# Kernel tuning notes

Hardware: AMD Instinct MI355X
Metric: run time of the kernel (lower is better)

Reference implementation:

```python
import jax, jax.numpy as jnp
import numpy as np

N_NODES = 50000
N_EDGES = 800000
N_GRAPHS = 500
NFEAT = 128
NHID = 64
NLAYER = 3
BN_EPS = 1e-5


def setup_inputs() -> dict:
    key = jax.random.key(0)
    ks = jax.random.split(key, 8)
    x = jax.random.normal(ks[0], (N_NODES, NFEAT), dtype=jnp.float32)
    edge_index = jax.random.randint(ks[1], (2, N_EDGES), 0, N_NODES)
    batch = jnp.sort(jax.random.randint(ks[2], (N_NODES,), 0, N_GRAPHS))
    Wt = jax.random.normal(ks[3], (NFEAT, NHID), dtype=jnp.float32) / np.float32(np.sqrt(NFEAT))
    bt = jnp.zeros((NHID,), jnp.float32)
    gamma0 = jnp.ones((NHID,), jnp.float32)
    beta0 = jnp.zeros((NHID,), jnp.float32)
    W1 = jax.random.normal(ks[4], (NLAYER, NHID, NHID), dtype=jnp.float32) / np.float32(np.sqrt(NHID))
    W2 = jax.random.normal(ks[5], (NLAYER, NHID, NHID), dtype=jnp.float32) / np.float32(np.sqrt(NHID))
    gammas = jnp.ones((NLAYER, NHID), jnp.float32)
    betas = jnp.zeros((NLAYER, NHID), jnp.float32)
    return dict(x=x, edge_index=edge_index, batch=batch, Wt=Wt, bt=bt,
                gamma0=gamma0, beta0=beta0, W1=W1, W2=W2, gammas=gammas, betas=betas)


def _bn(h, g, b):
    # BatchNorm1d training-mode math: batch mean, biased variance
    mean = jnp.mean(h, axis=0)
    var = jnp.mean((h - mean) ** 2, axis=0)
    return (h - mean) * jax.lax.rsqrt(var + BN_EPS) * g + b


def _pool_mean(h, batch):
    s = jax.ops.segment_sum(h, batch, num_segments=N_GRAPHS)
    cnt = jax.ops.segment_sum(jnp.ones((h.shape[0], 1), h.dtype), batch, num_segments=N_GRAPHS)
    return s / jnp.maximum(cnt, 1.0)


def _embed_std(h, batch):
    m = _pool_mean(h, batch)                      # [G, nhid]
    s = jnp.sqrt(_pool_mean((h - m[batch]) ** 2, batch))
    return m, s


def reference(x, edge_index, batch, Wt, bt, gamma0, beta0, W1, W2, gammas, betas):
    src, dst = edge_index[0], edge_index[1]
    h = _bn(x @ Wt + bt, gamma0, beta0)           # transform: Linear + BN
    e0, s0 = _embed_std(h, batch)

    def step(h, p):
        w1, w2, g, b = p
        agg = jax.ops.segment_sum(h[src], dst, num_segments=N_NODES)  # GIN sum-aggregation
        z = (h + agg)                              # (1+eps)*x + agg, eps=0
        z = jax.nn.relu(z @ w1) @ w2               # GINConv nn: Linear-ReLU-Linear (no bias)
        z = _bn(jax.nn.relu(z), g, b)              # act then BN
        e, s = _embed_std(z, batch)
        return z, (e, s)

    _, (es, ss) = jax.lax.scan(step, h, (W1, W2, gammas, betas))
    graph_embeds = jnp.concatenate([e0[None], es], axis=0)  # [nlayer+1, G, nhid]
    graph_stds = jnp.concatenate([s0[None], ss], axis=0)
    return graph_embeds, graph_stds
```

## Files before the change

### kernel.cpp

```cpp
#include <hip/hip_runtime.h>
#include <hip/hip_bf16.h>

#define NN 50000
#define NE 800000
#define NG 500
#define NF 128
#define NH 64
#define NB 256
#define NPB 196
#define EPB 4096
#define NBLK ((NE + EPB - 1)/EPB)
#define CSR_LDS 2048

typedef unsigned int u32;
typedef unsigned short u16;
typedef _Float16 h2 __attribute__((ext_vector_type(2)));
typedef _Float16 h8 __attribute__((ext_vector_type(8)));
typedef float f32x4 __attribute__((ext_vector_type(4)));

__device__ __forceinline__ float bf1(u16 v){ return __uint_as_float(((u32)v) << 16); }
__device__ __forceinline__ float h1(u16 v){ return (float)__builtin_bit_cast(_Float16, v); }
__device__ __forceinline__ u32 pk(float a, float b){
  return __builtin_bit_cast(u32, __builtin_amdgcn_cvt_pkrtz(a, b));
}
__device__ __forceinline__ h2 uph(u32 u){ return __builtin_bit_cast(h2, u); }
__device__ __forceinline__ u16 f16b(float f){ return __builtin_bit_cast(u16, (_Float16)f); }

__device__ __forceinline__ void cv8h(uint4 q, float* f){
  h2 v0 = uph(q.x), v1 = uph(q.y), v2 = uph(q.z), v3 = uph(q.w);
  f[0]=(float)v0.x; f[1]=(float)v0.y; f[2]=(float)v1.x; f[3]=(float)v1.y;
  f[4]=(float)v2.x; f[5]=(float)v2.y; f[6]=(float)v3.x; f[7]=(float)v3.y;
}

__device__ __forceinline__ h8 pack8(float4 p, float4 q){
  uint4 t;
  t.x = pk(p.x, p.y); t.y = pk(p.z, p.w);
  t.z = pk(q.x, q.y); t.w = pk(q.z, q.w);
  return __builtin_bit_cast(h8, t);
}
__device__ __forceinline__ f32x4 z4(){
  f32x4 v; v[0]=0.f; v[1]=0.f; v[2]=0.f; v[3]=0.f; return v;
}

__global__ __launch_bounds__(256) void k_init(const u32* __restrict__ xw, int* __restrict__ flag,
    const int* __restrict__ batch, int* __restrict__ starts,
    const float* __restrict__ Wt, const float* __restrict__ W1, const float* __restrict__ W2,
    u16* __restrict__ wtT, u16* __restrict__ w1T, u16* __restrict__ w2T){
  int b = blockIdx.x, tid = threadIdx.x;
  if (b < 48){
    int t = b*256 + tid;
    if (t < NH*NF){
      int c = t >> 7, k = t & 127;
      wtT[t] = f16b(Wt[(size_t)k*NH + c]);
    }
    if (t < 3*NH*NH){
      int l = t >> 12, c = (t >> 6) & 63, k = t & 63;
      w1T[t] = f16b(W1[(size_t)l*NH*NH + k*NH + c]);
      w2T[t] = f16b(W2[(size_t)l*NH*NH + k*NH + c]);
    }
  } else {
    if (tid < 64){
      u32 w = xw[tid];
      u32 lo = w & 0xFFFFu;
      u32 e = (lo >> 7) & 0xFFu;
      bool vote = (e >= 0x60u && e <= 0x8Fu);
      unsigned long long m = __ballot(vote);
      if (tid == 0) flag[0] = (__popcll(m) >= 32) ? 1 : 0;
    }
    for (int g = tid; g <= NG; g += 256){
      int lo = 0, hi = NN;
      while (lo < hi){ int mid = (lo + hi) >> 1; if (batch[mid] < g) lo = mid + 1; else hi = mid; }
      starts[g] = lo;
    }
  }
}


__global__ __launch_bounds__(256) void k_bhist(const int* __restrict__ ei, int* __restrict__ bcount,
    int* __restrict__ bstart, int* __restrict__ bcur, int* __restrict__ ticket){
  __shared__ int h[NB];
  __shared__ int part[NB];
  __shared__ int isLast;
  int tid = threadIdx.x;
  h[tid] = 0;
  __syncthreads();
  int e0 = blockIdx.x*EPB;
  #pragma unroll
  for (int i = 0; i < 16; i++){
    int e = e0 + i*256 + tid;
    if (e < NE) atomicAdd(&h[ei[NE + e] / NPB], 1);
  }
  __syncthreads();
  if (h[tid]) atomicAdd(&bcount[tid], h[tid]);
  __threadfence();
  if (tid == 0) isLast = (atomicAdd(ticket, 1) == (int)gridDim.x - 1);
  __syncthreads();
  if (!isLast) return;
  int v = atomicAdd(&bcount[tid], 0);
  part[tid] = v;
  __syncthreads();
  for (int off = 1; off < 256; off <<= 1){
    int u = (tid >= off) ? part[tid-off] : 0;
    __syncthreads();
    part[tid] += u;
    __syncthreads();
  }
  int ex = part[tid] - v;
  bstart[tid] = ex;
  bcur[tid] = ex;
  if (tid == 0) bstart[NB] = NE;
}

__global__ __launch_bounds__(256) void k_bscat(const int* __restrict__ ei,
    int* __restrict__ bcur, u32* __restrict__ pkE){
  __shared__ int h[NB];
  __shared__ int loff[NB];
  __shared__ int base[NB];
  __shared__ int part[NB];
  __shared__ u32 sv[EPB];
  int tid = threadIdx.x;
  h[tid] = 0;
  __syncthreads();
  int e0 = blockIdx.x*EPB;
  u32 meta[16], vals[16];
  #pragma unroll
  for (int i = 0; i < 16; i++){
    int e = e0 + i*256 + tid;
    if (e < NE){
      int s = ei[e], d = ei[NE + e];
      int b = d / NPB;
      int r = atomicAdd(&h[b], 1);
      meta[i] = ((u32)b << 16) | (u32)r;
      vals[i] = ((u32)d << 16) | (u32)s;
    } else meta[i] = 0xFFFFFFFFu;
  }
  __syncthreads();
  int cnt = h[tid];
  part[tid] = cnt;
  __syncthreads();
  for (int off = 1; off < 256; off <<= 1){
    int u = (tid >= off) ? part[tid-off] : 0;
    __syncthreads();
    part[tid] += u;
    __syncthreads();
  }
  loff[tid] = part[tid] - cnt;
  base[tid] = cnt ? atomicAdd(&bcur[tid], cnt) : 0;
  __syncthreads();
  #pragma unroll
  for (int i = 0; i < 16; i++){
    if (meta[i] != 0xFFFFFFFFu){
      int b = meta[i] >> 16, r = meta[i] & 0xFFFFu;
      sv[loff[b] + r] = vals[i];
    }
  }
  __syncthreads();
  int total = min(EPB, NE - e0);
  for (int j = tid; j < total; j += 256){
    u32 v = sv[j];
    int b = (int)(v >> 16) / NPB;
    pkE[base[b] + (j - loff[b])] = v;
  }
}

__global__ __launch_bounds__(256) void k_bfill(const u32* __restrict__ pkE,
    const int* __restrict__ bstart, int* __restrict__ rowptr, int* __restrict__ csr){
  __shared__ int part[NB];
  __shared__ int cur[NB];
  int b = blockIdx.x;
  int tid = threadIdx.x;
  int nb0 = b*NPB;
  int nr = min(NPB, NN - nb0);
  int rbeg = bstart[b], rend = bstart[b+1];
  part[tid] = 0;
  __syncthreads();
  for (int j = rbeg + tid; j < rend; j += 256){
    u32 pe = pkE[j];
    atomicAdd(&part[(int)(pe >> 16) - nb0], 1);
  }
  __syncthreads();
  int v = part[tid];
  __syncthreads();
  for (int off = 1; off < 256; off <<= 1){
    int u = (tid >= off) ? part[tid-off] : 0;
    __syncthreads();
    part[tid] += u;
    __syncthreads();
  }
  int ex = part[tid] - v;
  if (tid < nr) rowptr[nb0 + tid] = rbeg + ex;
  if (b == NB-1 && tid == 0) rowptr[NN] = NE;
  cur[tid] = ex;
  __syncthreads();
  for (int j = rbeg + tid; j < rend; j += 256){
    u32 pe = pkE[j];
    int node = (int)(pe >> 16) - nb0;
    int p = atomicAdd(&cur[node], 1);
    csr[rbeg + p] = (int)(pe & 0xFFFFu);
  }
}

__global__ __launch_bounds__(256) void k_transform_m(const float* __restrict__ x,
    const u16* __restrict__ wtT, const float* __restrict__ bt,
    u16* __restrict__ th, float* __restrict__ s1){
  __shared__ float sRed[8*NH];
  int tid = threadIdx.x;
  int w = tid >> 6, l = tid & 63;
  int lr = l & 15, kb = l >> 4;
  h8 bf[4][4];
  #pragma unroll
  for (int n = 0; n < 4; n++)
    #pragma unroll
    for (int kk = 0; kk < 4; kk++)
      bf[n][kk] = *(const h8*)&wtT[(size_t)(16*n + lr)*NF + kk*32 + kb*8];
  int node0 = blockIdx.x*64 + w*16;
  int rowA = node0 + lr; if (rowA > NN-1) rowA = NN-1;
  const float* xr = x + (size_t)rowA*NF + kb*8;
  f32x4 acc[4];
  #pragma unroll
  for (int n = 0; n < 4; n++) acc[n] = z4();
  #pragma unroll
  for (int kk = 0; kk < 4; kk++){
    float4 p = *(const float4*)(xr + kk*32);
    float4 q = *(const float4*)(xr + kk*32 + 4);
    h8 a = pack8(p, q);
    #pragma unroll
    for (int n = 0; n < 4; n++)
      acc[n] = __builtin_amdgcn_mfma_f32_16x16x32_f16(a, bf[n][kk], acc[n], 0, 0, 0);
  }
  #pragma unroll
  for (int n = 0; n < 4; n++){
    float bias = bt[16*n + lr];
    float a1 = 0.f, a2 = 0.f;
    #pragma unroll
    for (int r = 0; r < 4; r++){
      int g = node0 + 4*kb + r;
      float v = acc[n][r] + bias;
      if (g < NN){
        th[(size_t)g*NH + 16*n + lr] = f16b(v);
        a1 += v; a2 += v*v;
      }
    }
    a1 += __shfl_xor(a1, 16); a1 += __shfl_xor(a1, 32);
    a2 += __shfl_xor(a2, 16); a2 += __shfl_xor(a2, 32);
    if (kb == 0){
      sRed[w*NH + 16*n + lr] = a1;
      sRed[(4+w)*NH + 16*n + lr] = a2;
    }
  }
  __syncthreads();
  if (tid < NH){
    float a1 = sRed[tid] + sRed[NH+tid] + sRed[2*NH+tid] + sRed[3*NH+tid];
    float a2 = sRed[4*NH+tid] + sRed[5*NH+tid] + sRed[6*NH+tid] + sRed[7*NH+tid];
    unsafeAtomicAdd(&s1[tid], a1);
    unsafeAtomicAdd(&s1[NH+tid], a2);
  }
}

__global__ __launch_bounds__(512) void k_gmlp(const u16* __restrict__ t,
    const int* __restrict__ rowptr, const int* __restrict__ csr, u16* __restrict__ Th,
    const u16* __restrict__ w1T, const u16* __restrict__ w2T, int wofs,
    const float* __restrict__ s1i,
    const void* __restrict__ gamma, const void* __restrict__ beta, int ofs,
    const int* __restrict__ flag, float* __restrict__ s1o){
  __shared__ __align__(16) u16 sU[64*NH];
  __shared__ __align__(16) u16 sV[64*NH];
  __shared__ float sRed[8*NH];
  __shared__ float scs[NH], shs[NH];
  __shared__ int sCsr[CSR_LDS];
  __shared__ int sRp[65];
  int tid = threadIdx.x;
  int node0 = blockIdx.x*64;
  if (tid < NH){
    int bfl = flag[0];
    float gm = bfl ? bf1(((const u16*)gamma)[ofs+tid]) : ((const float*)gamma)[ofs+tid];
    float be = bfl ? bf1(((const u16*)beta)[ofs+tid])  : ((const float*)beta)[ofs+tid];
    float mean = s1i[tid] * (1.f/NN);
    float var  = s1i[NH+tid] * (1.f/NN) - mean*mean;
    float rr = rsqrtf(fmaxf(var, 0.f) + 1e-5f);
    float sc = gm * rr;
    scs[tid] = sc;
    shs[tid] = be - mean*sc;
  }
  if (tid >= 128 && tid < 193){
    int idx = tid - 128;
    int nd = node0 + idx;
    sRp[idx] = rowptr[nd > NN ? NN : nd];
  }
  __syncthreads();
  int base = sRp[0];
  int cnt = sRp[64] - base;
  for (int i = tid; i < cnt && i < CSR_LDS; i += 512) sCsr[i] = csr[base + i];
  __syncthreads();
  int w = tid >> 6, lane = tid & 63;
  int chunk = lane & 7, epar = lane >> 3;
  for (int idx = 0; idx < 8; idx++){
    int nl = w*8 + idx;
    int node = node0 + nl;
    int swz = (nl & 7) << 3;
    if (node < NN){
      int beg = sRp[nl], en = sRp[nl+1];
      float acc[8] = {0.f,0.f,0.f,0.f,0.f,0.f,0.f,0.f};
      if (epar == 0){
        uint4 q = *(const uint4*)&t[(size_t)node*NH + chunk*8];
        cv8h(q, acc);
      }
      int j = beg + epar;
      for (; j + 8 < en; j += 16){
        int o0 = j - base, o1 = o0 + 8;
        int src0 = (o0 < CSR_LDS) ? sCsr[o0] : csr[j];
        int src1 = (o1 < CSR_LDS) ? sCsr[o1] : csr[j+8];
        uint4 q0 = *(const uint4*)&t[(size_t)src0*NH + chunk*8];
        uint4 q1 = *(const uint4*)&t[(size_t)src1*NH + chunk*8];
        float f0[8], f1[8];
        cv8h(q0, f0);
        cv8h(q1, f1);
        #pragma unroll
        for (int i = 0; i < 8; i++) acc[i] += f0[i] + f1[i];
      }
      if (j < en){
        int o0 = j - base;
        int src = (o0 < CSR_LDS) ? sCsr[o0] : csr[j];
        uint4 q = *(const uint4*)&t[(size_t)src*NH + chunk*8];
        float f[8]; cv8h(q, f);
        #pragma unroll
        for (int i = 0; i < 8; i++) acc[i] += f[i];
      }
      #pragma unroll
      for (int i = 0; i < 8; i++){
        acc[i] += __shfl_xor(acc[i], 8);
        acc[i] += __shfl_xor(acc[i], 16);
        acc[i] += __shfl_xor(acc[i], 32);
      }
      if (epar == 0){
        float deg1 = (float)(en - beg + 1);
        float o[8];
        #pragma unroll
        for (int i = 0; i < 8; i++)
          o[i] = scs[chunk*8+i]*acc[i] + deg1*shs[chunk*8+i];
        uint4 ov;
        ov.x = pk(o[0], o[1]); ov.y = pk(o[2], o[3]);
        ov.z = pk(o[4], o[5]); ov.w = pk(o[6], o[7]);
        *(uint4*)&sU[nl*NH + ((chunk*8) ^ swz)] = ov;
      }
    } else if (epar == 0){
      uint4 zz; zz.x = 0; zz.y = 0; zz.z = 0; zz.w = 0;
      *(uint4*)&sU[nl*NH + ((chunk*8) ^ swz)] = zz;
    }
  }
  __syncthreads();
  int lr = lane & 15, kb = lane >> 4;
  int rb = w & 3, ch = w >> 2;
  h8 b1[2][2], b2[2][2];
  #pragma unroll
  for (int n2 = 0; n2 < 2; n2++)
    #pragma unroll
    for (int kk = 0; kk < 2; kk++){
      int n = 2*ch + n2;
      b1[n2][kk] = *(const h8*)&w1T[wofs + (16*n + lr)*NH + kk*32 + kb*8];
      b2[n2][kk] = *(const h8*)&w2T[wofs + (16*n + lr)*NH + kk*32 + kb*8];
    }
  int rv = 16*rb + lr;
  f32x4 acc[2];
  acc[0] = z4(); acc[1] = z4();
  const u16* urow = sU + rv*NH;
  #pragma unroll
  for (int kk = 0; kk < 2; kk++){
    h8 a = *(const h8*)&urow[(kk*32 + kb*8) ^ ((rv & 7) << 3)];
    #pragma unroll
    for (int n2 = 0; n2 < 2; n2++)
      acc[n2] = __builtin_amdgcn_mfma_f32_16x16x32_f16(a, b1[n2][kk], acc[n2], 0, 0, 0);
  }
  #pragma unroll
  for (int n2 = 0; n2 < 2; n2++){
    int n = 2*ch + n2;
    #pragma unroll
    for (int r = 0; r < 4; r++){
      int row = 16*rb + 4*kb + r;
      int col = 16*n + lr;
      sV[row*NH + (col ^ ((row & 7) << 3))] = f16b(fmaxf(acc[n2][r], 0.f));
    }
  }
  __syncthreads();
  f32x4 acc2[2];
  acc2[0] = z4(); acc2[1] = z4();
  const u16* vrow = sV + rv*NH;
  #pragma unroll
  for (int kk = 0; kk < 2; kk++){
    h8 a = *(const h8*)&vrow[(kk*32 + kb*8) ^ ((rv & 7) << 3)];
    #pragma unroll
    for (int n2 = 0; n2 < 2; n2++)
      acc2[n2] = __builtin_amdgcn_mfma_f32_16x16x32_f16(a, b2[n2][kk], acc2[n2], 0, 0, 0);
  }
  #pragma unroll
  for (int n2 = 0; n2 < 2; n2++){
    int n = 2*ch + n2;
    float a1 = 0.f, a2 = 0.f;
    #pragma unroll
    for (int r = 0; r < 4; r++){
      int g = node0 + 16*rb + 4*kb + r;
      float v = fmaxf(acc2[n2][r], 0.f);
      if (g < NN){
        Th[(size_t)g*NH + 16*n + lr] = f16b(v);
        a1 += v; a2 += v*v;
      }
    }
    a1 += __shfl_xor(a1, 16); a1 += __shfl_xor(a1, 32);
    a2 += __shfl_xor(a2, 16); a2 += __shfl_xor(a2, 32);
    if (kb == 0){
      sRed[rb*NH + 16*n + lr] = a1;
      sRed[(4+rb)*NH + 16*n + lr] = a2;
    }
  }
  __syncthreads();
  if (tid < NH){
    float a1 = sRed[tid] + sRed[NH+tid] + sRed[2*NH+tid] + sRed[3*NH+tid];
    float a2 = sRed[4*NH+tid] + sRed[5*NH+tid] + sRed[6*NH+tid] + sRed[7*NH+tid];
    unsafeAtomicAdd(&s1o[tid], a1);
    unsafeAtomicAdd(&s1o[NH+tid], a2);
  }
}

__global__ __launch_bounds__(512) void k_embed(const u16* __restrict__ t,
    const float* __restrict__ s1,
    const void* __restrict__ gamma, const void* __restrict__ beta, int ofs,
    const int* __restrict__ starts, const int* __restrict__ flag,
    void* __restrict__ dout, int layer){
  __shared__ float sRed[16*NH];
  int g = blockIdx.x;
  int tx = threadIdx.x & 63, ty = threadIdx.x >> 6;
  int bf = flag[0];
  float gm = bf ? bf1(((const u16*)gamma)[ofs+tx]) : ((const float*)gamma)[ofs+tx];
  float be = bf ? bf1(((const u16*)beta)[ofs+tx])  : ((const float*)beta)[ofs+tx];
  float mean = s1[tx] * (1.f/NN);
  float var  = s1[NH+tx] * (1.f/NN) - mean*mean;
  float rr = rsqrtf(fmaxf(var, 0.f) + 1e-5f);
  float sc = gm * rr;
  float sh = be - mean*sc;
  int st = starts[g], en = starts[g+1];
  float ls1 = 0.f, ls2 = 0.f;
  for (int n = st + ty; n < en; n += 8){
    float z = h1(t[(size_t)n*NH + tx]) * sc + sh;
    ls1 += z; ls2 += z*z;
  }
  sRed[ty*NH + tx] = ls1;
  sRed[(8+ty)*NH + tx] = ls2;
  __syncthreads();
  if (ty == 0){
    float a1 = 0.f, a2 = 0.f;
    #pragma unroll
    for (int r = 0; r < 8; r++){
      a1 += sRed[r*NH + tx];
      a2 += sRed[(8+r)*NH + tx];
    }
    int cnt = en - st;
    float inv = 1.f / (float)max(cnt, 1);
    float m = a1 * inv;
    float vv = a2 * inv - m*m;
    float s = sqrtf(fmaxf(vv, 0.f));
    size_t eidx = ((size_t)layer*NG + g)*NH + tx;
    size_t sidx = (size_t)4*NG*NH + eidx;
    if (bf){
      ((__hip_bfloat16*)dout)[eidx] = __float2bfloat16(m);
      ((__hip_bfloat16*)dout)[sidx] = __float2bfloat16(s);
    } else {
      ((float*)dout)[eidx] = m;
      ((float*)dout)[sidx] = s;
    }
  }
}

extern "C" void kernel_launch(void* const* d_in, const int* in_sizes, int n_in,
                              void* d_out, int out_size, void* d_ws, size_t ws_size,
                              hipStream_t stream) {
  const void* x    = d_in[0];
  const int* ei    = (const int*)d_in[1];
  const int* batch = (const int*)d_in[2];
  const void* Wt   = d_in[3];
  const void* bt   = d_in[4];
  const void* g0   = d_in[5];
  const void* b0   = d_in[6];
  const void* W1   = d_in[7];
  const void* W2   = d_in[8];
  const void* gs   = d_in[9];
  const void* bs   = d_in[10];

  u16*  tA    = (u16*)d_ws;
  u16*  tB    = tA + (size_t)NN*NH;
  float* sAll = (float*)(tB + (size_t)NN*NH);
  int* bcount = (int*)(sAll + 512);
  int* ticket = bcount + NB;
  int* bstart = ticket + 64;
  int* bcur   = bstart + 288;
  int* starts = bcur + NB;
  int* flag   = starts + 512;
  int* rowptr = flag + 64;
  u32* pkE    = (u32*)(rowptr + NN + 64);
  int* csr    = (int*)(pkE + NE);
  u16* wtT    = (u16*)(csr + NE);
  u16* w1T    = wtT + (size_t)NH*NF;
  u16* w2T    = w1T + (size_t)3*NH*NH;

  hipMemsetAsync(sAll, 0, (512 + NB + 64)*sizeof(float), stream);
  k_init<<<49, 256, 0, stream>>>((const u32*)x, flag, batch, starts,
      (const float*)Wt, (const float*)W1, (const float*)W2, wtT, w1T, w2T);
  k_bhist<<<NBLK, 256, 0, stream>>>(ei, bcount, bstart, bcur, ticket);
  k_bscat<<<NBLK, 256, 0, stream>>>(ei, bcur, pkE);
  k_bfill<<<NB, 256, 0, stream>>>(pkE, bstart, rowptr, csr);

  k_transform_m<<<(NN+63)/64, 256, 0, stream>>>((const float*)x, wtT, (const float*)bt, tA, sAll);
  k_embed<<<NG, 512, 0, stream>>>(tA, sAll, g0, b0, 0, starts, flag, d_out, 0);

  u16* tin = tA;
  u16* tout = tB;
  for (int l = 0; l < 3; l++){
    float* sIn  = sAll + (size_t)l*128;
    float* sOut = sAll + (size_t)(l+1)*128;
    const void* gg = (l == 0) ? g0 : gs;
    const void* bb = (l == 0) ? b0 : bs;
    int ofs = (l == 0) ? 0 : (l-1)*NH;
    k_gmlp<<<(NN+63)/64, 512, 0, stream>>>(tin, rowptr, csr, tout, w1T, w2T, l*NH*NH,
        sIn, gg, bb, ofs, flag, sOut);
    k_embed<<<NG, 512, 0, stream>>>(tout, sOut, gs, bs, l*NH, starts, flag, d_out, l+1);
    u16* tmp = tin; tin = tout; tout = tmp;
  }
}
```

Baseline: 332.9 us.

## Fuse per-graph embedding stats into GIN aggregation kernel and software-pipeline gathers

Per-graph mean and std of each layer's normalized input are now computed inside k_gmlp while it reads each node's own row. Partial sums go into shared-memory bins for the first few graphs a block touches, with global atomics as fallback, so three of the four k_embed launches and their extra passes over the node features go away. The neighbor gather is also unrolled and double-buffered across node pairs, issuing up to four neighbor loads ahead of consumption. The cost is more register pressure, extra LDS and atomics, a larger memset, and a sum-of-squares variance that may lose precision.

```diff
diff --git a/kernel.cpp b/kernel.cpp
--- a/kernel.cpp
+++ b/kernel.cpp
@@ -11,6 +11,7 @@
 #define EPB 4096
 #define NBLK ((NE + EPB - 1)/EPB)
 #define CSR_LDS 2048
+#define GBIN 6
 
 typedef unsigned int u32;
 typedef unsigned short u16;
@@ -257,18 +258,96 @@
   }
 }
 
+#define GISS(IDX, Q, QS, BEG, EN, GI) { \
+  int nl_ = w*8 + (IDX); \
+  int node_ = node0 + nl_; \
+  int valid_ = node_ < NN; \
+  BEG = valid_ ? sRp[nl_] : 0; \
+  EN  = valid_ ? sRp[nl_+1] : 0; \
+  int selfn_ = valid_ ? node_ : 0; \
+  GI = batch[selfn_]; \
+  QS = *(const uint4*)&t[(size_t)selfn_*NH + chunk*8]; \
+  _Pragma("unroll") \
+  for (int s_ = 0; s_ < 4; s_++){ \
+    int j_ = BEG + epar + 8*s_; \
+    int src_ = selfn_; \
+    if (j_ < EN){ int o_ = j_ - base; src_ = (o_ < CSR_LDS) ? sCsr[o_] : csr[j_]; } \
+    Q[s_] = *(const uint4*)&t[(size_t)src_*NH + chunk*8]; \
+  } }
+
+#define GCON(IDX, Q, QS, BEG, EN, GI) { \
+  int nl_ = w*8 + (IDX); \
+  int node_ = node0 + nl_; \
+  int valid_ = node_ < NN; \
+  int swz_ = (nl_ & 7) << 3; \
+  float acc_[8] = {0.f,0.f,0.f,0.f,0.f,0.f,0.f,0.f}; \
+  if (epar == 0 && valid_){ \
+    float sv_[8]; cv8h(QS, sv_); \
+    int gl_ = GI - gFirst; \
+    _Pragma("unroll") \
+    for (int i_ = 0; i_ < 8; i_++){ \
+      float z_ = scs[chunk*8+i_]*sv_[i_] + shs[chunk*8+i_]; \
+      acc_[i_] = sv_[i_]; \
+      if (gl_ >= 0 && gl_ < GBIN){ \
+        atomicAdd(&sGE[gl_*NH + chunk*8 + i_], z_); \
+        atomicAdd(&sGS[gl_*NH + chunk*8 + i_], z_*z_); \
+      } else { \
+        unsafeAtomicAdd(&gstatEL[(size_t)GI*NH + chunk*8 + i_], z_); \
+        unsafeAtomicAdd(&gstatSL[(size_t)GI*NH + chunk*8 + i_], z_*z_); \
+      } \
+    } \
+  } \
+  _Pragma("unroll") \
+  for (int s_ = 0; s_ < 4; s_++){ \
+    if (BEG + epar + 8*s_ < EN){ \
+      float f_[8]; cv8h(Q[s_], f_); \
+      _Pragma("unroll") for (int i_ = 0; i_ < 8; i_++) acc_[i_] += f_[i_]; \
+    } \
+  } \
+  for (int j_ = BEG + epar + 32; j_ < EN; j_ += 8){ \
+    int o_ = j_ - base; int src_ = (o_ < CSR_LDS) ? sCsr[o_] : csr[j_]; \
+    uint4 qq_ = *(const uint4*)&t[(size_t)src_*NH + chunk*8]; \
+    float f_[8]; cv8h(qq_, f_); \
+    _Pragma("unroll") for (int i_ = 0; i_ < 8; i_++) acc_[i_] += f_[i_]; \
+  } \
+  _Pragma("unroll") \
+  for (int i_ = 0; i_ < 8; i_++){ \
+    acc_[i_] += __shfl_xor(acc_[i_], 8); \
+    acc_[i_] += __shfl_xor(acc_[i_], 16); \
+    acc_[i_] += __shfl_xor(acc_[i_], 32); \
+  } \
+  if (epar == 0){ \
+    if (valid_){ \
+      float deg1_ = (float)(EN - BEG + 1); \
+      float o_[8]; \
+      _Pragma("unroll") \
+      for (int i_ = 0; i_ < 8; i_++) o_[i_] = scs[chunk*8+i_]*acc_[i_] + deg1_*shs[chunk*8+i_]; \
+      uint4 ov_; ov_.x = pk(o_[0], o_[1]); ov_.y = pk(o_[2], o_[3]); \
+      ov_.z = pk(o_[4], o_[5]); ov_.w = pk(o_[6], o_[7]); \
+      *(uint4*)&sU[nl_*NH + ((chunk*8) ^ swz_)] = ov_; \
+    } else { \
+      uint4 zz_; zz_.x = 0; zz_.y = 0; zz_.z = 0; zz_.w = 0; \
+      *(uint4*)&sU[nl_*NH + ((chunk*8) ^ swz_)] = zz_; \
+    } } }
+
 __global__ __launch_bounds__(512) void k_gmlp(const u16* __restrict__ t,
-    const int* __restrict__ rowptr, const int* __restrict__ csr, u16* __restrict__ Th,
+    const int* __restrict__ rowptr, const int* __restrict__ csr,
+    const int* __restrict__ batch, u16* __restrict__ Th,
     const u16* __restrict__ w1T, const u16* __restrict__ w2T, int wofs,
     const float* __restrict__ s1i,
     const void* __restrict__ gamma, const void* __restrict__ beta, int ofs,
-    const int* __restrict__ flag, float* __restrict__ s1o){
+    const int* __restrict__ flag, float* __restrict__ s1o, float* __restrict__ gstatL){
   __shared__ __align__(16) u16 sU[64*NH];
   __shared__ __align__(16) u16 sV[64*NH];
   __shared__ float sRed[8*NH];
   __shared__ float scs[NH], shs[NH];
   __shared__ int sCsr[CSR_LDS];
   __shared__ int sRp[65];
+  __shared__ float sGE[GBIN*NH];
+  __shared__ float sGS[GBIN*NH];
+  __shared__ int sGFirst;
+  float* gstatEL = gstatL;
+  float* gstatSL = gstatL + (size_t)NG*NH;
   int tid = threadIdx.x;
   int node0 = blockIdx.x*64;
   if (tid < NH){
@@ -287,76 +366,54 @@
     int nd = node0 + idx;
     sRp[idx] = rowptr[nd > NN ? NN : nd];
   }
+  if (tid < GBIN*NH){ sGE[tid] = 0.f; sGS[tid] = 0.f; }
+  if (tid == 200) sGFirst = batch[node0];
   __syncthreads();
   int base = sRp[0];
   int cnt = sRp[64] - base;
+  int gFirst = sGFirst;
   for (int i = tid; i < cnt && i < CSR_LDS; i += 512) sCsr[i] = csr[base + i];
   __syncthreads();
   int w = tid >> 6, lane = tid & 63;
   int chunk = lane & 7, epar = lane >> 3;
-  for (int idx = 0; idx < 8; idx++){
-    int nl = w*8 + idx;
-    int node = node0 + nl;
-    int swz = (nl & 7) << 3;
-    if (node < NN){
-      int beg = sRp[nl], en = sRp[nl+1];
-      float acc[8] = {0.f,0.f,0.f,0.f,0.f,0.f,0.f,0.f};
-      if (epar == 0){
-        uint4 q = *(const uint4*)&t[(size_t)node*NH + chunk*8];
-        cv8h(q, acc);
-      }
-      int j = beg + epar;
-      for (; j + 8 < en; j += 16){
-        int o0 = j - base, o1 = o0 + 8;
-        int src0 = (o0 < CSR_LDS) ? sCsr[o0] : csr[j];
-        int src1 = (o1 < CSR_LDS) ? sCsr[o1] : csr[j+8];
-        uint4 q0 = *(const uint4*)&t[(size_t)src0*NH + chunk*8];
-        uint4 q1 = *(const uint4*)&t[(size_t)src1*NH + chunk*8];
-        float f0[8], f1[8];
-        cv8h(q0, f0);
-        cv8h(q1, f1);
-        #pragma unroll
-        for (int i = 0; i < 8; i++) acc[i] += f0[i] + f1[i];
-      }
-      if (j < en){
-        int o0 = j - base;
-        int src = (o0 < CSR_LDS) ? sCsr[o0] : csr[j];
-        uint4 q = *(const uint4*)&t[(size_t)src*NH + chunk*8];
-        float f[8]; cv8h(q, f);
-        #pragma unroll
-        for (int i = 0; i < 8; i++) acc[i] += f[i];
-      }
-      #pragma unroll
-      for (int i = 0; i < 8; i++){
-        acc[i] += __shfl_xor(acc[i], 8);
-        acc[i] += __shfl_xor(acc[i], 16);
-        acc[i] += __shfl_xor(acc[i], 32);
-      }
-      if (epar == 0){
-        float deg1 = (float)(en - beg + 1);
-        float o[8];
-        #pragma unroll
-        for (int i = 0; i < 8; i++)
-          o[i] = scs[chunk*8+i]*acc[i] + deg1*shs[chunk*8+i];
-        uint4 ov;
-        ov.x = pk(o[0], o[1]); ov.y = pk(o[2], o[3]);
-        ov.z = pk(o[4], o[5]); ov.w = pk(o[6], o[7]);
-        *(uint4*)&sU[nl*NH + ((chunk*8) ^ swz)] = ov;
-      }
-    } else if (epar == 0){
-      uint4 zz; zz.x = 0; zz.y = 0; zz.z = 0; zz.w = 0;
-      *(uint4*)&sU[nl*NH + ((chunk*8) ^ swz)] = zz;
-    }
-  }
-  __syncthreads();
+  {
+    int begA, enA, giA, begB, enB, giB;
+    uint4 qA[4], qB[4], qsA, qsB;
+    GISS(0, qA, qsA, begA, enA, giA)
+    GISS(1, qB, qsB, begB, enB, giB)
+    GCON(0, qA, qsA, begA, enA, giA)
+    GISS(2, qA, qsA, begA, enA, giA)
+    GCON(1, qB, qsB, begB, enB, giB)
+    GISS(3, qB, qsB, begB, enB, giB)
+    GCON(2, qA, qsA, begA, enA, giA)
+    GISS(4, qA, qsA, begA, enA, giA)
+    GCON(3, qB, qsB, begB, enB, giB)
+    GISS(5, qB, qsB, begB, enB, giB)
+    GCON(4, qA, qsA, begA, enA, giA)
+    GISS(6, qA, qsA, begA, enA, giA)
+    GCON(5, qB, qsB, begB, enB, giB)
+    GISS(7, qB, qsB, begB, enB, giB)
+    GCON(6, qA, qsA, begA, enA, giA)
+    GCON(7, qB, qsB, begB, enB, giB)
+  }
+  __syncthreads();
+  if (tid < GBIN*NH){
+    int bin = tid >> 6, ch = tid & 63;
+    float vE = sGE[tid], vS = sGS[tid];
+    int g = gFirst + bin;
+    if (vE != 0.f || vS != 0.f){
+      unsafeAtomicAdd(&gstatEL[(size_t)g*NH + ch], vE);
+      unsafeAtomicAdd(&gstatSL[(size_t)g*NH + ch], vS);
+    }
+  }
   int lr = lane & 15, kb = lane >> 4;
-  int rb = w & 3, ch = w >> 2;
+  int rb = w & 3, ch2 = w >> 2;
   h8 b1[2][2], b2[2][2];
   #pragma unroll
   for (int n2 = 0; n2 < 2; n2++)
     #pragma unroll
     for (int kk = 0; kk < 2; kk++){
-      int n = 2*ch + n2;
+      int n = 2*ch2 + n2;
       b1[n2][kk] = *(const h8*)&w1T[wofs + (16*n + lr)*NH + kk*32 + kb*8];
       b2[n2][kk] = *(const h8*)&w2T[wofs + (16*n + lr)*NH + kk*32 + kb*8];
     }
@@ -373,7 +430,7 @@
   }
   #pragma unroll
   for (int n2 = 0; n2 < 2; n2++){
-    int n = 2*ch + n2;
+    int n = 2*ch2 + n2;
     #pragma unroll
     for (int r = 0; r < 4; r++){
       int row = 16*rb + 4*kb + r;
@@ -394,7 +451,7 @@
   }
   #pragma unroll
   for (int n2 = 0; n2 < 2; n2++){
-    int n = 2*ch + n2;
+    int n = 2*ch2 + n2;
     float a1 = 0.f, a2 = 0.f;
     #pragma unroll
     for (int r = 0; r < 4; r++){
@@ -425,7 +482,7 @@
     const float* __restrict__ s1,
     const void* __restrict__ gamma, const void* __restrict__ beta, int ofs,
     const int* __restrict__ starts, const int* __restrict__ flag,
-    void* __restrict__ dout, int layer){
+    void* __restrict__ dout, int layer, const float* __restrict__ gstat){
   __shared__ float sRed[16*NH];
   int g = blockIdx.x;
   int tx = threadIdx.x & 63, ty = threadIdx.x >> 6;
@@ -438,6 +495,25 @@
   float sc = gm * rr;
   float sh = be - mean*sc;
   int st = starts[g], en = starts[g+1];
+  int cnt = en - st;
+  float inv = 1.f / (float)max(cnt, 1);
+  if (threadIdx.x < 3*NH){
+    int l = threadIdx.x >> 6, ch = threadIdx.x & 63;
+    const float* gE = gstat + (size_t)l*2*NG*NH;
+    const float* gS = gE + (size_t)NG*NH;
+    float m = gE[(size_t)g*NH + ch] * inv;
+    float vv = gS[(size_t)g*NH + ch] * inv - m*m;
+    float s = sqrtf(fmaxf(vv, 0.f));
+    size_t eidx = ((size_t)l*NG + g)*NH + ch;
+    size_t sidx = (size_t)4*NG*NH + eidx;
+    if (bf){
+      ((__hip_bfloat16*)dout)[eidx] = __float2bfloat16(m);
+      ((__hip_bfloat16*)dout)[sidx] = __float2bfloat16(s);
+    } else {
+      ((float*)dout)[eidx] = m;
+      ((float*)dout)[sidx] = s;
+    }
+  }
   float ls1 = 0.f, ls2 = 0.f;
   for (int n = st + ty; n < en; n += 8){
     float z = h1(t[(size_t)n*NH + tx]) * sc + sh;
@@ -453,8 +529,6 @@
       a1 += sRed[r*NH + tx];
       a2 += sRed[(8+r)*NH + tx];
     }
-    int cnt = en - st;
-    float inv = 1.f / (float)max(cnt, 1);
     float m = a1 * inv;
     float vv = a2 * inv - m*m;
     float s = sqrtf(fmaxf(vv, 0.f));
@@ -490,7 +564,8 @@
   float* sAll = (float*)(tB + (size_t)NN*NH);
   int* bcount = (int*)(sAll + 512);
   int* ticket = bcount + NB;
-  int* bstart = ticket + 64;
+  float* gstat = (float*)(ticket + 64);
+  int* bstart = (int*)(gstat + (size_t)3*2*NG*NH);
   int* bcur   = bstart + 288;
   int* starts = bcur + NB;
   int* flag   = starts + 512;
@@ -501,7 +576,8 @@
   u16* w1T    = wtT + (size_t)NH*NF;
   u16* w2T    = w1T + (size_t)3*NH*NH;
 
-  hipMemsetAsync(sAll, 0, (512 + NB + 64)*sizeof(float), stream);
+  size_t zbytes = (512 + NB + 64)*sizeof(float) + (size_t)3*2*NG*NH*sizeof(float);
+  hipMemsetAsync(sAll, 0, zbytes, stream);
   k_init<<<49, 256, 0, stream>>>((const u32*)x, flag, batch, starts,
       (const float*)Wt, (const float*)W1, (const float*)W2, wtT, w1T, w2T);
   k_bhist<<<NBLK, 256, 0, stream>>>(ei, bcount, bstart, bcur, ticket);
@@ -509,7 +585,6 @@
   k_bfill<<<NB, 256, 0, stream>>>(pkE, bstart, rowptr, csr);
 
   k_transform_m<<<(NN+63)/64, 256, 0, stream>>>((const float*)x, wtT, (const float*)bt, tA, sAll);
-  k_embed<<<NG, 512, 0, stream>>>(tA, sAll, g0, b0, 0, starts, flag, d_out, 0);
 
   u16* tin = tA;
   u16* tout = tB;
@@ -519,9 +594,9 @@
     const void* gg = (l == 0) ? g0 : gs;
     const void* bb = (l == 0) ? b0 : bs;
     int ofs = (l == 0) ? 0 : (l-1)*NH;
-    k_gmlp<<<(NN+63)/64, 512, 0, stream>>>(tin, rowptr, csr, tout, w1T, w2T, l*NH*NH,
-        sIn, gg, bb, ofs, flag, sOut);
-    k_embed<<<NG, 512, 0, stream>>>(tout, sOut, gs, bs, l*NH, starts, flag, d_out, l+1);
+    k_gmlp<<<(NN+63)/64, 512, 0, stream>>>(tin, rowptr, csr, batch, tout, w1T, w2T, l*NH*NH,
+        sIn, gg, bb, ofs, flag, sOut, gstat + (size_t)l*2*NG*NH);
     u16* tmp = tin; tin = tout; tout = tmp;
   }
-}
+  k_embed<<<NG, 512, 0, stream>>>(tin, sAll + 384, gs, bs, 2*NH, starts, flag, d_out, 3, gstat);
+}
```

Measured after the change: 432.3 us. +29.9%, slower.
